# Kernel optimization log

Measured on AMD Instinct MI355X. Metric: run time of the kernel, lower is better.

## Reference

```python
import jax, jax.numpy as jnp
import numpy as np
from jax import lax

N_BITS = 4  # init kwarg n_bits
Q_SCALE = 2.0 ** (N_BITS - 1) - 1.0  # signed n-bit levels


def ste_round(x):
    # straight-through rounding (identity gradient)
    return x + lax.stop_gradient(jnp.round(x) - x)


def quant_signed(x):
    # clip to [-1,1], quantize to 2^(n-1)-1 signed levels with STE
    return ste_round(jnp.clip(x, -1.0, 1.0) * Q_SCALE) / Q_SCALE


def qconv(x, w):
    # QuantizeConv: 3x3 stride-1 pad-1 conv with n-bit quantized weights
    return lax.conv_general_dilated(x, quant_signed(w), window_strides=(1, 1),
                                    padding=((1, 1), (1, 1)),
                                    dimension_numbers=('NCHW', 'OIHW', 'NCHW'))


def qact_conv(x, g, b):
    # QuantizeSignedActSBN (conv): per-channel scale/bias then signed quant
    return quant_signed(x * g[None, :, None, None] + b[None, :, None, None])


def qact_fc(x, g, b):
    return quant_signed(x * g[None, :] + b[None, :])


def maxpool2(x):
    return lax.reduce_window(x, -jnp.inf, lax.max, (1, 1, 2, 2), (1, 1, 2, 2), 'VALID')


def setup_inputs() -> dict:
    key = jax.random.key(0)
    ks = jax.random.split(key, 32)
    B = 512
    x = jax.random.normal(ks[0], (B, 3, 32, 32), dtype=jnp.float32)
    chans = [(64, 3), (64, 64), (128, 64), (128, 128), (256, 128), (256, 256)]
    inp = {'x': x}
    ki = 1
    for i, (co, ci) in enumerate(chans, start=1):
        inp[f'w{i}'] = jax.random.normal(ks[ki], (co, ci, 3, 3), dtype=jnp.float32) * 0.05; ki += 1
        inp[f'g{i}'] = jax.random.uniform(ks[ki], (co,), dtype=jnp.float32, minval=0.5, maxval=1.5); ki += 1
        inp[f'b{i}'] = jax.random.normal(ks[ki], (co,), dtype=jnp.float32) * 0.05; ki += 1
    # FC head: 4096 -> 512 -> 10 (torch Linear weight layout [out, in])
    inp['wf1'] = jax.random.normal(ks[ki], (512, 4096), dtype=jnp.float32) * 0.02; ki += 1
    inp['gf1'] = jax.random.uniform(ks[ki], (512,), dtype=jnp.float32, minval=0.5, maxval=1.5); ki += 1
    inp['bf1'] = jax.random.normal(ks[ki], (512,), dtype=jnp.float32) * 0.05; ki += 1
    inp['wf2'] = jax.random.normal(ks[ki], (10, 512), dtype=jnp.float32) * 0.05; ki += 1
    inp['gf2'] = jax.random.uniform(ks[ki], (10,), dtype=jnp.float32, minval=0.5, maxval=1.5); ki += 1
    inp['bf2'] = jax.random.normal(ks[ki], (10,), dtype=jnp.float32) * 0.05; ki += 1
    return inp


def reference(x, w1, g1, b1, w2, g2, b2, w3, g3, b3, w4, g4, b4, w5, g5, b5, w6, g6, b6,
              wf1, gf1, bf1, wf2, gf2, bf2):
    h = jax.nn.relu(qact_conv(qconv(x, w1), g1, b1))
    h = jax.nn.relu(qact_conv(qconv(h, w2), g2, b2))
    h = maxpool2(h)  # 32 -> 16
    h = jax.nn.relu(qact_conv(qconv(h, w3), g3, b3))
    h = jax.nn.relu(qact_conv(qconv(h, w4), g4, b4))
    h = maxpool2(h)  # 16 -> 8
    h = jax.nn.relu(qact_conv(qconv(h, w5), g5, b5))
    h = jax.nn.relu(qact_conv(qconv(h, w6), g6, b6))
    h = maxpool2(h)  # 8 -> 4 => 256*4*4 = 4096
    h = h.reshape(h.shape[0], -1)
    h = jax.nn.relu(qact_fc(h @ quant_signed(wf1).T, gf1, bf1))
    h = qact_fc(h @ quant_signed(wf2).T, gf2, bf2)
    return h
```

## Files before the change

kernel.cpp:

```cpp
#include <hip/hip_runtime.h>


typedef __attribute__((ext_vector_type(4))) int v4i;

#if defined(__has_builtin)
# if __has_builtin(__builtin_amdgcn_sdot4)
#  define HAS_SDOT4 1
# endif
#endif

__device__ __forceinline__ int dot4_i8(int a, int b, int c) {
#ifdef HAS_SDOT4
    return __builtin_amdgcn_sdot4(a, b, c, false);
#else
    c += ((a      ) & 0xff) * (int)(signed char)(b      );
    c += ((a >>  8) & 0xff) * (int)(signed char)(b >>  8);
    c += ((a >> 16) & 0xff) * (int)(signed char)(b >> 16);
    c += ((a >> 24) & 0xff) * (int)(signed char)(b >> 24);
    return c;
#endif
}

__device__ __forceinline__ void gld_lds16(const void* g, void* l) {
    __builtin_amdgcn_global_load_lds(
        (const __attribute__((address_space(1))) unsigned int*)g,
        (__attribute__((address_space(3))) unsigned int*)l, 16, 0, 0);
}

#define O_QW1D   0u
#define O_QWF2   14336u
#define O_ZERO   19456u
#define O_QWT2   24576u
#define O_QWT3   65536u
#define O_QWT4   147456u
#define O_QWT5   294912u
#define O_QWT6   589824u
#define O_QWF1   1179648u
#define O_BUFA   3276800u
#define O_BUFB   36831232u

__device__ __forceinline__ signed char quant_wf(float v) {
    return (signed char)(int)rintf(fminf(fmaxf(v, -1.0f), 1.0f) * 7.0f);
}

__device__ __forceinline__ void quantw1_body(const float* __restrict__ w,
                                             double* __restrict__ q, int i, int n) {
    if (i < n) q[i] = (double)quant_wf(w[i]);
}

__device__ __forceinline__ void quantw_body(const float* __restrict__ w,
                                            signed char* __restrict__ q, int i, int n) {
    if (i < n) q[i] = quant_wf(w[i]);
}

__device__ __forceinline__ void quantw_t8p_body(const float* __restrict__ w,
                                                signed char* __restrict__ o,
                                                int CI, int i, int n) {
    if (i < n) {
        const int b  = i & 15;
        const int t  = i >> 4;
        const int rows_per_grp = CI * 36;
        const int grp  = t / rows_per_grp;
        int rr = t - grp * rows_per_grp;
        const int pass = rr / 2304;
        rr -= pass * 2304;
        const int c    = rr / 576;
        const int row  = rr - c * 576;
        const int co_l = row / 9;
        const int tap  = row - co_l * 9;
        const int co = grp * 64 + co_l;
        const int ci = pass * 64 + c * 16 + b;
        o[i] = quant_wf(w[(co * CI + ci) * 9 + tap]);
    }
}

__device__ __forceinline__ void quantw_fc1_row(const float* __restrict__ w,
                                               signed char* __restrict__ o,
                                               int row, int tid,
                                               unsigned char* __restrict__ sb)
{
    const float4* wr = (const float4*)(w + row * 4096);
    unsigned int* so = (unsigned int*)sb;
#pragma unroll
    for (int k = 0; k < 4; ++k) {
        const int d = k * 256 + tid;
        float4 v = wr[d];
        unsigned int pk =
              ((unsigned int)(unsigned char)quant_wf(v.x))
            | ((unsigned int)(unsigned char)quant_wf(v.y) << 8)
            | ((unsigned int)(unsigned char)quant_wf(v.z) << 16)
            | ((unsigned int)(unsigned char)quant_wf(v.w) << 24);
        so[d] = pk;
    }
    __syncthreads();
    unsigned int* og = (unsigned int*)(o + row * 4096);
#pragma unroll
    for (int k = 0; k < 4; ++k) {
        const int od = k * 256 + tid;
        unsigned int pk = 0;
#pragma unroll
        for (int u = 0; u < 4; ++u) {
            const int kn = od * 4 + u;
            const int gp = kn >> 8, r = kn & 255;
            const int px = r >> 4, b = r & 15;
            const int ko = (gp * 16 + b) * 16 + px;
            pk |= (unsigned int)sb[ko] << (8 * u);
        }
        og[od] = pk;
    }
}

__global__ __launch_bounds__(256) void prep_k(
    const float* __restrict__ w1,  double* __restrict__ qw1d,
    const float* __restrict__ wf2, signed char* __restrict__ qwf2,
    const float* __restrict__ w2,  signed char* __restrict__ qwt2,
    const float* __restrict__ w3,  signed char* __restrict__ qwt3,
    const float* __restrict__ w4,  signed char* __restrict__ qwt4,
    const float* __restrict__ w5,  signed char* __restrict__ qwt5,
    const float* __restrict__ w6,  signed char* __restrict__ qwt6,
    const float* __restrict__ wf1, signed char* __restrict__ qwf1,
    unsigned char* __restrict__ zs)
{
    __shared__ __align__(16) unsigned char sb[4096];
    const int blk = blockIdx.x;
    const int t   = threadIdx.x;
    if (blk == 0 && t < 16) ((int4*)zs)[t] = int4{0, 0, 0, 0};
    if      (blk < 7)    quantw1_body(w1, qw1d, blk * 256 + t, 1728);
    else if (blk < 27)   quantw_body(wf2, qwf2, (blk - 7) * 256 + t, 5120);
    else if (blk < 171)  quantw_t8p_body(w2, qwt2, 64,  (blk - 27)   * 256 + t, 36864);
    else if (blk < 459)  quantw_t8p_body(w3, qwt3, 64,  (blk - 171)  * 256 + t, 73728);
    else if (blk < 1035) quantw_t8p_body(w4, qwt4, 128, (blk - 459)  * 256 + t, 147456);
    else if (blk < 2187) quantw_t8p_body(w5, qwt5, 128, (blk - 1035) * 256 + t, 294912);
    else if (blk < 4491) quantw_t8p_body(w6, qwt6, 256, (blk - 2187) * 256 + t, 589824);
    else                 quantw_fc1_row(wf1, qwf1, blk - 4491, t, sb);
}

#define XSTR 34
#define XPL  (10 * XSTR)
__global__ __launch_bounds__(256) void conv1_k(
    const float* __restrict__ x, const double* __restrict__ wqd,
    const float* __restrict__ gvec, const float* __restrict__ bvec,
    unsigned char* __restrict__ out)
{
    __shared__ double xs[3 * XPL];
    __shared__ __align__(16) unsigned char ob[2][256 * 16];

    const int tid  = threadIdx.x;
    const int sp   = tid & 63;
    const int cg   = tid >> 6;
    const int img  = blockIdx.x >> 2;
    const int slab = blockIdx.x & 3;
    const int y0s  = slab * 8;
    const int yb = sp >> 4, xb = sp & 15;
    const int ysl = yb * 2, x0 = xb * 2;

    const int cgu = __builtin_amdgcn_readfirstlane(cg);
    const double* wb = wqd + cgu * 108;

    for (int i = tid; i < 3 * XPL; i += 256) {
        int ci = i / XPL, r = i - ci * XPL;
        int ry = r / XSTR, rx = r - ry * XSTR;
        int gy = y0s - 1 + ry, gx = rx - 1;
        double v = 0.0;
        if ((unsigned)gy < 32u && (unsigned)gx < 32u)
            v = (double)x[(img * 3 + ci) * 1024 + gy * 32 + gx];
        xs[i] = v;
    }
    __syncthreads();

    for (int cog = 0; cog < 4; ++cog) {
        double acc[4][4];
#pragma unroll
        for (int l = 0; l < 4; ++l)
#pragma unroll
            for (int p = 0; p < 4; ++p) acc[l][p] = 0.0;

#pragma unroll
        for (int ci = 0; ci < 3; ++ci) {
            double a[4][4];
#pragma unroll
            for (int iy = 0; iy < 4; ++iy)
#pragma unroll
                for (int ix = 0; ix < 4; ++ix)
                    a[iy][ix] = xs[ci * XPL + (ysl + iy) * XSTR + (x0 + ix)];
#pragma unroll
            for (int l = 0; l < 4; ++l) {
                const double* wr = wb + cog * 432 + l * 27 + ci * 9;
#pragma unroll
                for (int ky = 0; ky < 3; ++ky)
#pragma unroll
                    for (int kx = 0; kx < 3; ++kx) {
                        const double wv = wr[ky * 3 + kx];
                        acc[l][0] = fma(wv, a[ky    ][kx    ], acc[l][0]);
                        acc[l][1] = fma(wv, a[ky    ][kx + 1], acc[l][1]);
                        acc[l][2] = fma(wv, a[ky + 1][kx    ], acc[l][2]);
                        acc[l][3] = fma(wv, a[ky + 1][kx + 1], acc[l][3]);
                    }
            }
        }

        int qv[4][4];
#pragma unroll
        for (int l = 0; l < 4; ++l) {
            const int co = cog * 16 + cg * 4 + l;
            const double gg  = (double)gvec[co];
            const double bb7 = (double)bvec[co] * 7.0;
#pragma unroll
            for (int p = 0; p < 4; ++p) {
                int qi = (int)rint(fma(acc[l][p], gg, bb7));
                qv[l][p] = qi < 0 ? 0 : (qi > 7 ? 7 : qi);
            }
        }
#pragma unroll
        for (int p = 0; p < 4; ++p) {
            unsigned int wv = (unsigned int)qv[0][p]
                            | ((unsigned int)qv[1][p] << 8)
                            | ((unsigned int)qv[2][p] << 16)
                            | ((unsigned int)qv[3][p] << 24);
            const int r = ysl + (p >> 1), c = x0 + (p & 1);
            const int px = r * 32 + c;
            const int slot = (cg ^ ((px >> 3) & 3) ^ ((px >> 6) & 3)) & 3;
            *(unsigned int*)&ob[cog & 1][px * 16 + slot * 4] = wv;
        }
        __syncthreads();
        {
            uint4 d = *(const uint4*)&ob[cog & 1][tid * 16];
            const int s = (((tid >> 3) & 3) ^ ((tid >> 6) & 3)) & 3;
            unsigned e0 = d.x, e1 = d.y, e2 = d.z, e3 = d.w, t;
            if (s & 1) { t = e0; e0 = e1; e1 = t; t = e2; e2 = e3; e3 = t; }
            if (s & 2) { t = e0; e0 = e2; e2 = t; t = e1; e1 = e3; e3 = t; }
            uint4 o; o.x = e0; o.y = e1; o.z = e2; o.w = e3;
            *(uint4*)&out[(size_t)img * 65536 + (size_t)cog * 16384
                          + y0s * 512 + tid * 16] = o;
        }
    }
}

template<int CI, int CO, int H, int W, bool POOL, int IPB, int TPB>
__global__ __launch_bounds__(256, 2) void conv_i8_k(
    const unsigned char* __restrict__ in, const signed char* __restrict__ wt,
    const float* __restrict__ gvec, const float* __restrict__ bvec,
    unsigned char* __restrict__ out, const unsigned char* __restrict__ zs)
{
    constexpr int ATX    = (IPB == 1) ? 18 : 10;
    constexpr int APX    = ATX * ATX;
    constexpr int APLANE = IPB * APX * 16;
    constexpr int AREG   = 4 * APLANE;
    constexpr int NBUF   = (TPB > 1) ? 2 : 1;
    constexpr int WBASE  = NBUF * AREG;
    constexpr int WPLANE = 576 * 16;
    constexpr int NPASS  = CI / 64;
    constexpr int PIN    = CI / 16;
    constexpr int PXI    = H * W;
    constexpr int POUT   = CO / 16;
    constexpr int PXO    = POOL ? (H / 2) * (W / 2) : H * W;
    static_assert(TPB == 1 || (NPASS == 1 && IPB == 1), "TPB>1 needs NPASS==1");

    __shared__ __align__(16) char lds[WBASE + 4 * WPLANE];

    const int tid = threadIdx.x;
    const int l   = tid & 63;
    const int w   = tid >> 6;
    const int n   = l & 15;
    const int q   = l >> 4;

    const int co_base = blockIdx.y * 64;
    const int wy8 = (IPB == 1) ? (w >> 1) * 8 : 0;
    const int wx8 = (IPB == 1) ? (w & 1) * 8 : 0;
    const int tilepx = (IPB == 4) ? w * APX : 0;

    const int ly = ((n >> 3) & 1) * 2 + ((n >> 1) & 1);
    const int lx = ((n >> 2) & 1) * 2 + (n & 1);

    int abase[4], wbase[4];
#pragma unroll
    for (int ps = 0; ps < 4; ++ps) {
        int ay0 = wy8 + (ps >> 1) * 4 + ly;
        int ax0 = wx8 + (ps & 1) * 4 + lx;
        abase[ps] = q * APLANE + (tilepx + ay0 * ATX + ax0) * 16;
    }
#pragma unroll
    for (int cs = 0; cs < 4; ++cs)
        wbase[cs] = WBASE + q * WPLANE + ((cs * 16 + n) * 9) * 16;

    auto stage_act = [&](int boff, int img0, int regY0, int regX0, int pass) {
#pragma unroll
        for (int c = 0; c < 4; ++c) {
            const int gp = pass * 4 + c;
            for (int base = 0; base < IPB * APX; base += 256) {
                const int px_g = base + tid;
                if (px_g < IPB * APX) {
                    int tile = 0, px = px_g;
                    if (IPB == 4) { tile = px_g / APX; px = px_g - tile * APX; }
                    const int gy = regY0 - 1 + px / ATX;
                    const int gx = regX0 - 1 + px % ATX;
                    const int bimg = img0 + tile;
                    const void* src =
                        ((unsigned)gy < (unsigned)H && (unsigned)gx < (unsigned)W)
                        ? (const void*)&in[((size_t)(bimg * PIN + gp) * PXI + gy * W + gx) * 16]
                        : (const void*)zs;
                    gld_lds16(src, &lds[boff + c * APLANE + px_g * 16]);
                }
            }
        }
    };
    auto stage_w = [&](int pass) {
        const signed char* wsrc = wt + (size_t)(blockIdx.y * NPASS + pass) * (4 * WPLANE);
#pragma unroll
        for (int base = 0; base < 2304; base += 256)
            gld_lds16(wsrc + (base + tid) * 16, &lds[WBASE + (base + tid) * 16]);
    };
    auto taps = [&](v4i acc[4][4], int boff) {
#pragma unroll
        for (int tap = 0; tap < 9; ++tap) {
            const int toff = ((tap / 3) * ATX + (tap % 3)) * 16;
            v4i bf[4], af[4];
#pragma unroll
            for (int cs = 0; cs < 4; ++cs)
                bf[cs] = *(const v4i*)&lds[wbase[cs] + tap * 16];
#pragma unroll
            for (int ps = 0; ps < 4; ++ps)
                af[ps] = *(const v4i*)&lds[boff + abase[ps] + toff];
#pragma unroll
            for (int ps = 0; ps < 4; ++ps)
#pragma unroll
                for (int cs = 0; cs < 4; ++cs)
                    acc[ps][cs] = __builtin_amdgcn_mfma_i32_16x16x64_i8(
                        af[ps], bf[cs], acc[ps][cs], 0, 0, 0);
        }
    };
    auto epilogue = [&](v4i acc[4][4], int img0, int regY0, int regX0) {
        const int bimg = (IPB == 1) ? img0 : (img0 + w);
#pragma unroll
        for (int cs = 0; cs < 4; ++cs) {
            const int co = co_base + cs * 16 + n;
            const int pl = (co_base >> 4) + cs;
            const double g7 = (double)gvec[co] * (1.0 / 7.0);
            const double b7 = (double)bvec[co] * 7.0;
#pragma unroll
            for (int ps = 0; ps < 4; ++ps) {
                const int Yb = regY0 + wy8 + (ps >> 1) * 4 + (q >> 1) * 2;
                const int Xb = regX0 + wx8 + (ps & 1) * 4 + (q & 1) * 2;
                if (POOL) {
                    int ms = max(max(acc[ps][cs][0], acc[ps][cs][1]),
                                 max(acc[ps][cs][2], acc[ps][cs][3]));
                    int qi = (int)rint(fma((double)ms, g7, b7));
                    qi = qi < 0 ? 0 : (qi > 7 ? 7 : qi);
                    out[((size_t)(bimg * POUT + pl) * PXO + (Yb >> 1) * (W / 2) + (Xb >> 1)) * 16 + n]
                        = (unsigned char)qi;
                } else {
#pragma unroll
                    for (int r = 0; r < 4; ++r) {
                        int qi = (int)rint(fma((double)acc[ps][cs][r], g7, b7));
                        qi = qi < 0 ? 0 : (qi > 7 ? 7 : qi);
                        const int Y = Yb + (r >> 1), X = Xb + (r & 1);
                        out[((size_t)(bimg * POUT + pl) * PXO + Y * W + X) * 16 + n]
                            = (unsigned char)qi;
                    }
                }
            }
        }
    };

    if (TPB == 1) {
        int img = 0, regY0 = 0, regX0 = 0;
        if (IPB == 1) {
            constexpr int rpw = W / 16;
            constexpr int rpi = (H / 16) * rpw;
            img   = blockIdx.x / rpi;
            int r = blockIdx.x % rpi;
            regY0 = (r / rpw) * 16;
            regX0 = (r % rpw) * 16;
        } else {
            img = (int)blockIdx.x * 4;
        }
        v4i acc[4][4];
#pragma unroll
        for (int ps = 0; ps < 4; ++ps)
#pragma unroll
            for (int cs = 0; cs < 4; ++cs) acc[ps][cs] = (v4i)0;

        for (int pass = 0; pass < NPASS; ++pass) {
            __syncthreads();
            stage_act(0, img, regY0, regX0, pass);
            stage_w(pass);
            __syncthreads();
            taps(acc, 0);
        }
        epilogue(acc, img, regY0, regX0);
    } else {
        auto tilec = [&](int t, int& im, int& ry, int& rx) {
            if (H == 32) { im = t >> 2; ry = ((t >> 1) & 1) * 16; rx = (t & 1) * 16; }
            else         { im = t; ry = 0; rx = 0; }
        };
        stage_w(0);
        int im0, ry0, rx0;
        tilec((int)blockIdx.x * TPB, im0, ry0, rx0);
        stage_act(0, im0, ry0, rx0, 0);
        __syncthreads();
        for (int tt = 0; tt < TPB; ++tt) {
            int imc, ryc, rxc;
            tilec((int)blockIdx.x * TPB + tt, imc, ryc, rxc);
            if (tt + 1 < TPB) {
                int imn, ryn, rxn;
                tilec((int)blockIdx.x * TPB + tt + 1, imn, ryn, rxn);
                stage_act(((tt + 1) & 1) * AREG, imn, ryn, rxn, 0);
            }
            v4i acc[4][4];
#pragma unroll
            for (int ps = 0; ps < 4; ++ps)
#pragma unroll
                for (int cs = 0; cs < 4; ++cs) acc[ps][cs] = (v4i)0;
            taps(acc, (tt & 1) * AREG);
            epilogue(acc, imc, ryc, rxc);
            __syncthreads();
        }
    }
}

__global__ __launch_bounds__(256, 2) void fc1_i8_k(
    const unsigned char* __restrict__ h, const signed char* __restrict__ wt,
    const float* __restrict__ gvec, const float* __restrict__ bvec,
    unsigned char* __restrict__ out)
{
    __shared__ int red[4096];
    const int tid = threadIdx.x;
    const int l = tid & 63, w = tid >> 6;
    const int n = l & 15, q = l >> 4;
    const int m0 = blockIdx.x * 32, n0 = blockIdx.y * 32;

    v4i acc[2][2];
#pragma unroll
    for (int a = 0; a < 2; ++a)
#pragma unroll
        for (int b = 0; b < 2; ++b) acc[a][b] = (v4i)0;

    const int kb = w * 1024;
    for (int ks = 0; ks < 16; ++ks) {
        const int k = kb + ks * 64 + q * 16;
        v4i af[2], bf[2];
#pragma unroll
        for (int ms = 0; ms < 2; ++ms)
            af[ms] = *(const v4i*)&h[(m0 + ms * 16 + n) * 4096 + k];
#pragma unroll
        for (int ns = 0; ns < 2; ++ns)
            bf[ns] = *(const v4i*)&wt[(n0 + ns * 16 + n) * 4096 + k];
#pragma unroll
        for (int ms = 0; ms < 2; ++ms)
#pragma unroll
            for (int ns = 0; ns < 2; ++ns)
                acc[ms][ns] = __builtin_amdgcn_mfma_i32_16x16x64_i8(
                    af[ms], bf[ns], acc[ms][ns], 0, 0, 0);
    }

#pragma unroll
    for (int ms = 0; ms < 2; ++ms)
#pragma unroll
        for (int ns = 0; ns < 2; ++ns)
#pragma unroll
            for (int r = 0; r < 4; ++r)
                red[w * 1024 + (ms * 16 + q * 4 + r) * 32 + ns * 16 + n] = acc[ms][ns][r];
    __syncthreads();

#pragma unroll
    for (int j = 0; j < 4; ++j) {
        const int e = tid * 4 + j;
        int s = red[e] + red[1024 + e] + red[2048 + e] + red[3072 + e];
        const int ml = e >> 5, nl = e & 31;
        const int co = n0 + nl;
        double y7 = fma((double)s, (double)gvec[co] * (1.0 / 7.0), (double)bvec[co] * 7.0);
        int qi = (int)rint(y7);
        qi = qi < 0 ? 0 : (qi > 7 ? 7 : qi);
        out[(m0 + ml) * 512 + co] = (unsigned char)qi;
    }
}

__global__ __launch_bounds__(256) void fc2_k(
    const unsigned char* __restrict__ h, const signed char* __restrict__ wq,
    const float* __restrict__ gvec, const float* __restrict__ bvec,
    float* __restrict__ out)
{
    const int gid = blockIdx.x * 256 + threadIdx.x;
    const int b = gid >> 4;
    const int n = gid & 15;
    if (b >= 512 || n >= 10) return;
    const int* hp = (const int*)&h[b * 512];
    const int* wp = (const int*)&wq[n * 512];
    int s = 0;
#pragma unroll 4
    for (int k = 0; k < 128; k += 4) {
        int4 hv = *(const int4*)&hp[k];
        int4 wv = *(const int4*)&wp[k];
        s = dot4_i8(hv.x, wv.x, s);
        s = dot4_i8(hv.y, wv.y, s);
        s = dot4_i8(hv.z, wv.z, s);
        s = dot4_i8(hv.w, wv.w, s);
    }
    double y7 = fma((double)s, (double)gvec[n] * (1.0 / 7.0), (double)bvec[n] * 7.0);
    double r = rint(y7);
    r = fmin(fmax(r, -7.0), 7.0);
    out[b * 10 + n] = (float)(r / 7.0);
}

extern "C" void kernel_launch(void* const* d_in, const int* in_sizes, int n_in,
                              void* d_out, int out_size, void* d_ws, size_t ws_size,
                              hipStream_t stream) {
    const float* x   = (const float*)d_in[0];
    const float* w1  = (const float*)d_in[1];
    const float* g1  = (const float*)d_in[2];
    const float* b1  = (const float*)d_in[3];
    const float* w2  = (const float*)d_in[4];
    const float* g2  = (const float*)d_in[5];
    const float* b2  = (const float*)d_in[6];
    const float* w3  = (const float*)d_in[7];
    const float* g3  = (const float*)d_in[8];
    const float* b3  = (const float*)d_in[9];
    const float* w4  = (const float*)d_in[10];
    const float* g4  = (const float*)d_in[11];
    const float* b4  = (const float*)d_in[12];
    const float* w5  = (const float*)d_in[13];
    const float* g5  = (const float*)d_in[14];
    const float* b5  = (const float*)d_in[15];
    const float* w6  = (const float*)d_in[16];
    const float* g6  = (const float*)d_in[17];
    const float* b6  = (const float*)d_in[18];
    const float* wf1 = (const float*)d_in[19];
    const float* gf1 = (const float*)d_in[20];
    const float* bf1 = (const float*)d_in[21];
    const float* wf2 = (const float*)d_in[22];
    const float* gf2 = (const float*)d_in[23];
    const float* bf2 = (const float*)d_in[24];

    char* ws = (char*)d_ws;
    double*        qw1d = (double*)(ws + O_QW1D);
    signed char*   qwf2 = (signed char*)(ws + O_QWF2);
    unsigned char* zs   = (unsigned char*)(ws + O_ZERO);
    signed char*   qwt2 = (signed char*)(ws + O_QWT2);
    signed char*   qwt3 = (signed char*)(ws + O_QWT3);
    signed char*   qwt4 = (signed char*)(ws + O_QWT4);
    signed char*   qwt5 = (signed char*)(ws + O_QWT5);
    signed char*   qwt6 = (signed char*)(ws + O_QWT6);
    signed char*   qwf1 = (signed char*)(ws + O_QWF1);
    unsigned char* bufA = (unsigned char*)(ws + O_BUFA);
    unsigned char* bufB = (unsigned char*)(ws + O_BUFB);

    hipLaunchKernelGGL(prep_k, dim3(5003), dim3(256), 0, stream,
                       w1, qw1d, wf2, qwf2, w2, qwt2, w3, qwt3,
                       w4, qwt4, w5, qwt5, w6, qwt6, wf1, qwf1, zs);

    hipLaunchKernelGGL(conv1_k, dim3(2048), dim3(256), 0, stream, x, qw1d, g1, b1, bufA);
    hipLaunchKernelGGL((conv_i8_k<64,  64,  32, 32, true,  1, 4>), dim3(512,  1), dim3(256), 0, stream, bufA, qwt2, g2, b2, bufB, zs);
    hipLaunchKernelGGL((conv_i8_k<64,  128, 16, 16, false, 1, 2>), dim3(256,  2), dim3(256), 0, stream, bufB, qwt3, g3, b3, bufA, zs);
    hipLaunchKernelGGL((conv_i8_k<128, 128, 16, 16, true,  1, 1>), dim3(512,  2), dim3(256), 0, stream, bufA, qwt4, g4, b4, bufB, zs);
    hipLaunchKernelGGL((conv_i8_k<128, 256, 8,  8,  false, 4, 1>), dim3(128,  4), dim3(256), 0, stream, bufB, qwt5, g5, b5, bufA, zs);
    hipLaunchKernelGGL((conv_i8_k<256, 256, 8,  8,  true,  4, 1>), dim3(128,  4), dim3(256), 0, stream, bufA, qwt6, g6, b6, bufB, zs);

    hipLaunchKernelGGL(fc1_i8_k, dim3(16, 16), dim3(256), 0, stream, bufB, qwf1, gf1, bf1, bufA);
    hipLaunchKernelGGL(fc2_k, dim3(32), dim3(256), 0, stream, bufA, qwf2, gf2, bf2, (float*)d_out);
}
```

Baseline: 241.4 us.

## Add specialized conv4 kernel splitting output channels into 32-wide groups with multi-tile blocks

Adds a new int8 MFMA conv kernel for the 128->128 16x16 pooled layer. Each block keeps the weights for 32 output channels resident in LDS and loops over four image tiles. The input-channel passes are double-buffered, with staging of the next pass overlapped with compute. This replaces the previous launch of 512x2 blocks with 128x4 blocks, aiming for more weight reuse and fewer weight reloads, at the cost of less parallelism per block and a different LDS footprint.

```diff
diff --git a/kernel.cpp b/kernel.cpp
--- a/kernel.cpp
+++ b/kernel.cpp
@@ -415,6 +415,159 @@
             epilogue(acc, imc, ryc, rxc);
             __syncthreads();
         }
+    }
+}
+
+template<int CI, int CO, int H, int W, bool POOL, int TPB>
+__global__ __launch_bounds__(256, 2) void conv_i8_fk(
+    const unsigned char* __restrict__ in, const signed char* __restrict__ wt,
+    const float* __restrict__ gvec, const float* __restrict__ bvec,
+    unsigned char* __restrict__ out, const unsigned char* __restrict__ zs)
+{
+    constexpr int ATX    = 18;
+    constexpr int APX    = 324;
+    constexpr int APLANE = APX * 16;
+    constexpr int AREG   = 4 * APLANE;
+    constexpr int WBASE  = 2 * AREG;
+    constexpr int WSEG   = 288 * 16;
+    constexpr int WPASS  = 4 * WSEG;
+    constexpr int NPASS  = CI / 64;
+    constexpr int PIN    = CI / 16;
+    constexpr int PXI    = H * W;
+    constexpr int POUT   = CO / 16;
+    constexpr int PXO    = POOL ? (H / 2) * (W / 2) : H * W;
+    static_assert(H == 16 && W == 16, "fk path: 16x16 tiles only");
+
+    __shared__ __align__(16) char lds[WBASE + NPASS * WPASS];
+
+    const int tid = threadIdx.x;
+    const int l   = tid & 63;
+    const int w   = tid >> 6;
+    const int n   = l & 15;
+    const int q   = l >> 4;
+
+    const int grp64 = blockIdx.y >> 1;
+    const int h     = blockIdx.y & 1;
+    const int co32  = blockIdx.y * 32;
+    const int wy8 = (w >> 1) * 8, wx8 = (w & 1) * 8;
+
+    const int ly = ((n >> 3) & 1) * 2 + ((n >> 1) & 1);
+    const int lx = ((n >> 2) & 1) * 2 + (n & 1);
+
+    int abase[4], wb2[2];
+#pragma unroll
+    for (int ps = 0; ps < 4; ++ps) {
+        int ay0 = wy8 + (ps >> 1) * 4 + ly;
+        int ax0 = wx8 + (ps & 1) * 4 + lx;
+        abase[ps] = (ay0 * ATX + ax0) * 16;
+    }
+#pragma unroll
+    for (int cs = 0; cs < 2; ++cs)
+        wb2[cs] = WBASE + q * WSEG + ((cs * 16 + n) * 9) * 16;
+
+    {
+        for (int i = tid; i < NPASS * 4 * 288; i += 256) {
+            const int pc = i / 288, r = i - pc * 288;
+            const int p = pc >> 2, c = pc & 3;
+            const signed char* src = wt
+                + (((size_t)(grp64 * NPASS + p) * 4 + c) * 576 + h * 288 + r) * 16;
+            gld_lds16(src, &lds[WBASE + i * 16]);
+        }
+    }
+    auto stage_act = [&](int boff, int img0, int pass) {
+#pragma unroll
+        for (int c = 0; c < 4; ++c) {
+            const int gp = pass * 4 + c;
+            for (int base = 0; base < APX; base += 256) {
+                const int px = base + tid;
+                if (px < APX) {
+                    const int gy = -1 + px / ATX;
+                    const int gx = -1 + px % ATX;
+                    const void* src =
+                        ((unsigned)gy < (unsigned)H && (unsigned)gx < (unsigned)W)
+                        ? (const void*)&in[((size_t)(img0 * PIN + gp) * PXI + gy * W + gx) * 16]
+                        : (const void*)zs;
+                    gld_lds16(src, &lds[boff + c * APLANE + px * 16]);
+                }
+            }
+        }
+    };
+
+    v4i acc[4][2];
+#pragma unroll
+    for (int ps = 0; ps < 4; ++ps)
+#pragma unroll
+        for (int cs = 0; cs < 2; ++cs) acc[ps][cs] = (v4i)0;
+
+    const int t0 = (int)blockIdx.x * TPB;
+    stage_act(0, t0, 0);
+    __syncthreads();
+
+    const int NS = TPB * NPASS;
+    for (int s = 0; s < NS; ++s) {
+        const int tile = s / NPASS, pass = s - tile * NPASS;
+        if (s + 1 < NS) {
+            const int tn = (s + 1) / NPASS, pn = (s + 1) - tn * NPASS;
+            stage_act(((s + 1) & 1) * AREG, t0 + tn, pn);
+        }
+        {
+            const int aoff = (s & 1) * AREG + q * APLANE;
+            const int woff = pass * WPASS;
+#pragma unroll
+            for (int tap = 0; tap < 9; ++tap) {
+                const int toff = ((tap / 3) * ATX + (tap % 3)) * 16;
+                v4i bf[2], af[4];
+#pragma unroll
+                for (int cs = 0; cs < 2; ++cs)
+                    bf[cs] = *(const v4i*)&lds[woff + wb2[cs] + tap * 16];
+#pragma unroll
+                for (int ps = 0; ps < 4; ++ps)
+                    af[ps] = *(const v4i*)&lds[aoff + abase[ps] + toff];
+#pragma unroll
+                for (int ps = 0; ps < 4; ++ps)
+#pragma unroll
+                    for (int cs = 0; cs < 2; ++cs)
+                        acc[ps][cs] = __builtin_amdgcn_mfma_i32_16x16x64_i8(
+                            af[ps], bf[cs], acc[ps][cs], 0, 0, 0);
+            }
+        }
+        if (pass == NPASS - 1) {
+            const int img = t0 + tile;
+#pragma unroll
+            for (int cs = 0; cs < 2; ++cs) {
+                const int co = co32 + cs * 16 + n;
+                const int pl = blockIdx.y * 2 + cs;
+                const double g7 = (double)gvec[co] * (1.0 / 7.0);
+                const double b7 = (double)bvec[co] * 7.0;
+#pragma unroll
+                for (int ps = 0; ps < 4; ++ps) {
+                    const int Yb = wy8 + (ps >> 1) * 4 + (q >> 1) * 2;
+                    const int Xb = wx8 + (ps & 1) * 4 + (q & 1) * 2;
+                    if (POOL) {
+                        int ms = max(max(acc[ps][cs][0], acc[ps][cs][1]),
+                                     max(acc[ps][cs][2], acc[ps][cs][3]));
+                        int qi = (int)rint(fma((double)ms, g7, b7));
+                        qi = qi < 0 ? 0 : (qi > 7 ? 7 : qi);
+                        out[((size_t)(img * POUT + pl) * PXO + (Yb >> 1) * (W / 2) + (Xb >> 1)) * 16 + n]
+                            = (unsigned char)qi;
+                    } else {
+#pragma unroll
+                        for (int r = 0; r < 4; ++r) {
+                            int qi = (int)rint(fma((double)acc[ps][cs][r], g7, b7));
+                            qi = qi < 0 ? 0 : (qi > 7 ? 7 : qi);
+                            const int Y = Yb + (r >> 1), X = Xb + (r & 1);
+                            out[((size_t)(img * POUT + pl) * PXO + Y * W + X) * 16 + n]
+                                = (unsigned char)qi;
+                        }
+                    }
+                }
+            }
+#pragma unroll
+            for (int ps = 0; ps < 4; ++ps)
+#pragma unroll
+                for (int cs = 0; cs < 2; ++cs) acc[ps][cs] = (v4i)0;
+        }
+        __syncthreads();
     }
 }
 
@@ -551,7 +704,7 @@
     hipLaunchKernelGGL(conv1_k, dim3(2048), dim3(256), 0, stream, x, qw1d, g1, b1, bufA);
     hipLaunchKernelGGL((conv_i8_k<64,  64,  32, 32, true,  1, 4>), dim3(512,  1), dim3(256), 0, stream, bufA, qwt2, g2, b2, bufB, zs);
     hipLaunchKernelGGL((conv_i8_k<64,  128, 16, 16, false, 1, 2>), dim3(256,  2), dim3(256), 0, stream, bufB, qwt3, g3, b3, bufA, zs);
-    hipLaunchKernelGGL((conv_i8_k<128, 128, 16, 16, true,  1, 1>), dim3(512,  2), dim3(256), 0, stream, bufA, qwt4, g4, b4, bufB, zs);
+    hipLaunchKernelGGL((conv_i8_fk<128, 128, 16, 16, true, 4>),    dim3(128,  4), dim3(256), 0, stream, bufA, qwt4, g4, b4, bufB, zs);
     hipLaunchKernelGGL((conv_i8_k<128, 256, 8,  8,  false, 4, 1>), dim3(128,  4), dim3(256), 0, stream, bufB, qwt5, g5, b5, bufA, zs);
     hipLaunchKernelGGL((conv_i8_k<256, 256, 8,  8,  true,  4, 1>), dim3(128,  4), dim3(256), 0, stream, bufA, qwt6, g6, b6, bufB, zs);
 
```

New measurement: 243.3 us. Within noise of the previous version (+0.8%).

## Compute conv1 in fp32 with fp64 recompute near rounding boundaries

Applied to the files above, without the earlier changes.

Switches the first convolution from double-precision to single-precision FMAs and LDS storage, which cuts both the FP64 arithmetic and the shared-memory footprint. To keep quantization exact, it computes an error bound from per-channel absolute weight sums and the maximum input magnitude. Outputs whose value lands within that bound of a rounding boundary are recomputed in double. This adds a divergent fallback path and a small prep step that writes the weight abs-sums.

```diff
diff --git a/kernel.cpp b/kernel.cpp
--- a/kernel.cpp
+++ b/kernel.cpp
@@ -27,7 +27,8 @@
         (__attribute__((address_space(3))) unsigned int*)l, 16, 0, 0);
 }
 
-#define O_QW1D   0u
+#define O_QW1F   0u
+#define O_WSAB   7168u
 #define O_QWF2   14336u
 #define O_ZERO   19456u
 #define O_QWT2   24576u
@@ -43,9 +44,9 @@
     return (signed char)(int)rintf(fminf(fmaxf(v, -1.0f), 1.0f) * 7.0f);
 }
 
-__device__ __forceinline__ void quantw1_body(const float* __restrict__ w,
-                                             double* __restrict__ q, int i, int n) {
-    if (i < n) q[i] = (double)quant_wf(w[i]);
+__device__ __forceinline__ void quantw1f_body(const float* __restrict__ w,
+                                              float* __restrict__ q, int i, int n) {
+    if (i < n) q[i] = (float)quant_wf(w[i]);
 }
 
 __device__ __forceinline__ void quantw_body(const float* __restrict__ w,
@@ -111,7 +112,8 @@
 }
 
 __global__ __launch_bounds__(256) void prep_k(
-    const float* __restrict__ w1,  double* __restrict__ qw1d,
+    const float* __restrict__ w1,  float* __restrict__ qw1f,
+    float* __restrict__ sabs,
     const float* __restrict__ wf2, signed char* __restrict__ qwf2,
     const float* __restrict__ w2,  signed char* __restrict__ qwt2,
     const float* __restrict__ w3,  signed char* __restrict__ qwt3,
@@ -125,7 +127,13 @@
     const int blk = blockIdx.x;
     const int t   = threadIdx.x;
     if (blk == 0 && t < 16) ((int4*)zs)[t] = int4{0, 0, 0, 0};
-    if      (blk < 7)    quantw1_body(w1, qw1d, blk * 256 + t, 1728);
+    if (blk == 0 && t < 64) {
+        float s = 0.0f;
+        for (int k = 0; k < 27; ++k)
+            s += fabsf((float)quant_wf(w1[t * 27 + k]));
+        sabs[t] = s;
+    }
+    if      (blk < 7)    quantw1f_body(w1, qw1f, blk * 256 + t, 1728);
     else if (blk < 27)   quantw_body(wf2, qwf2, (blk - 7) * 256 + t, 5120);
     else if (blk < 171)  quantw_t8p_body(w2, qwt2, 64,  (blk - 27)   * 256 + t, 36864);
     else if (blk < 459)  quantw_t8p_body(w3, qwt3, 64,  (blk - 171)  * 256 + t, 73728);
@@ -138,11 +146,12 @@
 #define XSTR 34
 #define XPL  (10 * XSTR)
 __global__ __launch_bounds__(256) void conv1_k(
-    const float* __restrict__ x, const double* __restrict__ wqd,
+    const float* __restrict__ x, const float* __restrict__ wqf,
+    const float* __restrict__ sabs,
     const float* __restrict__ gvec, const float* __restrict__ bvec,
     unsigned char* __restrict__ out)
 {
-    __shared__ double xs[3 * XPL];
+    __shared__ float xs[3 * XPL];
     __shared__ __align__(16) unsigned char ob[2][256 * 16];
 
     const int tid  = threadIdx.x;
@@ -155,46 +164,55 @@
     const int ysl = yb * 2, x0 = xb * 2;
 
     const int cgu = __builtin_amdgcn_readfirstlane(cg);
-    const double* wb = wqd + cgu * 108;
+    const float* wb = wqf + cgu * 108;
 
     for (int i = tid; i < 3 * XPL; i += 256) {
         int ci = i / XPL, r = i - ci * XPL;
         int ry = r / XSTR, rx = r - ry * XSTR;
         int gy = y0s - 1 + ry, gx = rx - 1;
-        double v = 0.0;
+        float v = 0.0f;
         if ((unsigned)gy < 32u && (unsigned)gx < 32u)
-            v = (double)x[(img * 3 + ci) * 1024 + gy * 32 + gx];
+            v = x[(img * 3 + ci) * 1024 + gy * 32 + gx];
         xs[i] = v;
     }
     __syncthreads();
 
+    float maxa = 0.0f;
+
     for (int cog = 0; cog < 4; ++cog) {
-        double acc[4][4];
+        float acc[4][4];
 #pragma unroll
         for (int l = 0; l < 4; ++l)
 #pragma unroll
-            for (int p = 0; p < 4; ++p) acc[l][p] = 0.0;
+            for (int p = 0; p < 4; ++p) acc[l][p] = 0.0f;
 
 #pragma unroll
         for (int ci = 0; ci < 3; ++ci) {
-            double a[4][4];
+            float a[4][4];
 #pragma unroll
             for (int iy = 0; iy < 4; ++iy)
 #pragma unroll
                 for (int ix = 0; ix < 4; ++ix)
                     a[iy][ix] = xs[ci * XPL + (ysl + iy) * XSTR + (x0 + ix)];
+            if (cog == 0) {
+#pragma unroll
+                for (int iy = 0; iy < 4; ++iy)
+#pragma unroll
+                    for (int ix = 0; ix < 4; ++ix)
+                        maxa = fmaxf(maxa, fabsf(a[iy][ix]));
+            }
 #pragma unroll
             for (int l = 0; l < 4; ++l) {
-                const double* wr = wb + cog * 432 + l * 27 + ci * 9;
+                const float* wr = wb + cog * 432 + l * 27 + ci * 9;
 #pragma unroll
                 for (int ky = 0; ky < 3; ++ky)
 #pragma unroll
                     for (int kx = 0; kx < 3; ++kx) {
-                        const double wv = wr[ky * 3 + kx];
-                        acc[l][0] = fma(wv, a[ky    ][kx    ], acc[l][0]);
-                        acc[l][1] = fma(wv, a[ky    ][kx + 1], acc[l][1]);
-                        acc[l][2] = fma(wv, a[ky + 1][kx    ], acc[l][2]);
-                        acc[l][3] = fma(wv, a[ky + 1][kx + 1], acc[l][3]);
+                        const float wv = wr[ky * 3 + kx];
+                        acc[l][0] = fmaf(wv, a[ky    ][kx    ], acc[l][0]);
+                        acc[l][1] = fmaf(wv, a[ky    ][kx + 1], acc[l][1]);
+                        acc[l][2] = fmaf(wv, a[ky + 1][kx    ], acc[l][2]);
+                        acc[l][3] = fmaf(wv, a[ky + 1][kx + 1], acc[l][3]);
                     }
             }
         }
@@ -205,9 +223,26 @@
             const int co = cog * 16 + cg * 4 + l;
             const double gg  = (double)gvec[co];
             const double bb7 = (double)bvec[co] * 7.0;
+            const double tau = (double)sabs[co] * (double)maxa * 4.0e-6 * gg + 1.0e-9;
 #pragma unroll
             for (int p = 0; p < 4; ++p) {
-                int qi = (int)rint(fma(acc[l][p], gg, bb7));
+                double y7 = fma((double)acc[l][p], gg, bb7);
+                double rn = rint(y7);
+                if (0.5 - fabs(y7 - rn) < tau) {
+                    double s = 0.0;
+                    const int dy = p >> 1, dx = p & 1;
+                    for (int ci = 0; ci < 3; ++ci) {
+                        const float* wr = wb + cog * 432 + l * 27 + ci * 9;
+                        for (int ky = 0; ky < 3; ++ky)
+                            for (int kx = 0; kx < 3; ++kx)
+                                s = fma((double)wr[ky * 3 + kx],
+                                        (double)xs[ci * XPL + (ysl + dy + ky) * XSTR
+                                                   + (x0 + dx + kx)], s);
+                    }
+                    y7 = fma(s, gg, bb7);
+                    rn = rint(y7);
+                }
+                int qi = (int)rn;
                 qv[l][p] = qi < 0 ? 0 : (qi > 7 ? 7 : qi);
             }
         }
@@ -532,7 +567,8 @@
     const float* bf2 = (const float*)d_in[24];
 
     char* ws = (char*)d_ws;
-    double*        qw1d = (double*)(ws + O_QW1D);
+    float*         qw1f = (float*)(ws + O_QW1F);
+    float*         sabs = (float*)(ws + O_WSAB);
     signed char*   qwf2 = (signed char*)(ws + O_QWF2);
     unsigned char* zs   = (unsigned char*)(ws + O_ZERO);
     signed char*   qwt2 = (signed char*)(ws + O_QWT2);
@@ -545,10 +581,10 @@
     unsigned char* bufB = (unsigned char*)(ws + O_BUFB);
 
     hipLaunchKernelGGL(prep_k, dim3(5003), dim3(256), 0, stream,
-                       w1, qw1d, wf2, qwf2, w2, qwt2, w3, qwt3,
+                       w1, qw1f, sabs, wf2, qwf2, w2, qwt2, w3, qwt3,
                        w4, qwt4, w5, qwt5, w6, qwt6, wf1, qwf1, zs);
 
-    hipLaunchKernelGGL(conv1_k, dim3(2048), dim3(256), 0, stream, x, qw1d, g1, b1, bufA);
+    hipLaunchKernelGGL(conv1_k, dim3(2048), dim3(256), 0, stream, x, qw1f, sabs, g1, b1, bufA);
     hipLaunchKernelGGL((conv_i8_k<64,  64,  32, 32, true,  1, 4>), dim3(512,  1), dim3(256), 0, stream, bufA, qwt2, g2, b2, bufB, zs);
     hipLaunchKernelGGL((conv_i8_k<64,  128, 16, 16, false, 1, 2>), dim3(256,  2), dim3(256), 0, stream, bufB, qwt3, g3, b3, bufA, zs);
     hipLaunchKernelGGL((conv_i8_k<128, 128, 16, 16, true,  1, 1>), dim3(512,  2), dim3(256), 0, stream, bufA, qwt4, g4, b4, bufB, zs);
```

After: 258.8 us. 7.2% more time.
